# Performance work log

Hardware: AMD Instinct MI355X
Metric: run time of the kernel (lower is better)

Reference implementation:

```python
import jax, jax.numpy as jnp
import numpy as np

H, W, CIN, COUT, B = 56, 56, 64, 64, 32
K = 3            # kernel_size
WIN = 15         # win_range
R = (WIN - 1) // 2


def _make_sample_idx():
    """Per-pixel fixed random sample locations within a WINxWIN window,
    mirroring Dconv_drop.__init__ (random.sample over valid window indices)."""
    rng = np.random.default_rng(0)
    ii = np.arange(H)[:, None, None]          # [H,1,1]
    jj = np.arange(W)[None, :, None]          # [1,W,1]
    lo_i = np.maximum(0, ii - R); hi_i = np.minimum(H - 1, ii + R)
    lo_j = np.maximum(0, jj - R); hi_j = np.minimum(W - 1, jj + R)
    ri = rng.integers(np.broadcast_to(lo_i, (H, W, K * K)),
                      np.broadcast_to(hi_i, (H, W, K * K)) + 1)
    rj = rng.integers(np.broadcast_to(lo_j, (H, W, K * K)),
                      np.broadcast_to(hi_j, (H, W, K * K)) + 1)
    return (ri * W + rj).astype(np.int32)    # [H,W,9] indices into H*W


def setup_inputs() -> dict:
    key = jax.random.key(0)
    k1, k2 = jax.random.split(key)
    x = jax.random.normal(k1, (B, CIN, H, W), dtype=jnp.float32)
    weight = jax.random.normal(k2, (COUT, CIN, K, K), dtype=jnp.float32) * 0.05
    sample_idx = jnp.asarray(_make_sample_idx())
    return {"x": x, "weight": weight, "sample_idx": sample_idx}


def reference(x, weight, sample_idx):
    # x: [B,C,H,W]; sample_idx: [H,W,9] flat indices into H*W.
    # Original: scatter gathered pixels into [B,C,3H,3W] grid, then
    # stride-3 kernel-3 conv => per-pixel contraction over the 9 samples.
    b, c, h, w = x.shape
    x_flat = x.reshape(b, c, h * w)
    gathered = x_flat[:, :, sample_idx]              # [B,C,H,W,9]
    w_flat = weight.reshape(weight.shape[0], c, K * K)  # [O,C,9]
    out = jnp.einsum('bchwk,ock->bohw', gathered, w_flat)
    return out
```

## Files before the change

kernel.cpp:

```cpp
#include <hip/hip_runtime.h>
#include <hip/hip_bf16.h>

#define HH 56
#define WW 56
#define CIN 64
#define COUT 64
#define BATCH 32
#define KK 9
#define HWP (HH*WW)
#define NS 18
#define NTILE 49
#define NBLK (NTILE*BATCH)
#define XT_OFF 73728
#define XSW 33

typedef __attribute__((ext_vector_type(8))) short short8;
typedef __attribute__((ext_vector_type(4))) float float4v;
typedef __attribute__((ext_vector_type(4))) unsigned int uint4v;

__device__ __forceinline__ unsigned short f2bf(float f) {
    union { float f; unsigned u; } v; v.f = f;
    unsigned r = v.u + 0x7FFFu + ((v.u >> 16) & 1u);
    return (unsigned short)(r >> 16);
}

__device__ __forceinline__ void prepack_elem(const float* __restrict__ w,
                                             unsigned short* __restrict__ apack,
                                             int e) {
    int j = e & 7;
    int l = (e >> 3) & 63;
    int ss = e >> 9;
    int mb = ss / 18;
    int s  = ss - mb * 18;
    int o = mb * 16 + (l & 15);
    int c = ((s & 1) << 5) + ((l >> 4) << 3) + j;
    int k = s >> 1;
    apack[e] = f2bf(w[(o * CIN + c) * KK + k]);
}

__global__ __launch_bounds__(256) void prep_kernel(
    const float* __restrict__ x, const float* __restrict__ w,
    unsigned int* __restrict__ xt, unsigned short* __restrict__ apack)
{
    int bid = blockIdx.x;
    int t   = threadIdx.x;
    if (bid < 784) {
        int u   = bid * 256 + t;
        int c2q = u & 7;
        int hq  = u >> 3;
        int b   = hq / 784;
        int q   = hq - b * 784;
        int hw  = q * 4;
        const float* xb = x + ((size_t)b * CIN + c2q * 8) * HWP + hw;
        float4v f[8];
        #pragma unroll
        for (int i = 0; i < 8; ++i)
            f[i] = *(const float4v*)(xb + (size_t)i * HWP);
        unsigned int* xto = xt + ((size_t)b * HWP + hw) * 32 + c2q * 4;
        #pragma unroll
        for (int j = 0; j < 4; ++j) {
            uint4v o;
            #pragma unroll
            for (int ci = 0; ci < 4; ++ci)
                o[ci] = (unsigned)f2bf(f[2 * ci][j]) |
                        ((unsigned)f2bf(f[2 * ci + 1][j]) << 16);
            *(uint4v*)(xto + (size_t)j * 32) = o;
        }
    } else {
        prepack_elem(w, apack, (bid - 784) * 256 + t);
    }
}

__global__ __launch_bounds__(256) void prep_weights_only(
    const float* __restrict__ w, unsigned short* __restrict__ apack)
{
    prepack_elem(w, apack, blockIdx.x * 256 + threadIdx.x);
}

__global__ __launch_bounds__(256, 5) void dconv_main(
    const unsigned int* __restrict__ xt, const int* __restrict__ sidx,
    const unsigned short* __restrict__ apack, float* __restrict__ out)
{
    __shared__ unsigned int xs[496 * 16];

    const int t    = threadIdx.x;
    const int lane = t & 63;
    const int wv   = t >> 6;
    const int mbp  = wv >> 1;
    const int ntp  = wv & 1;
    const int col  = lane & 15;
    const int krow = lane >> 4;

    int bid  = blockIdx.x;
    int orig = (bid & 7) * 196 + (bid >> 3);
    int b    = orig / NTILE;
    int bx   = orig - b * NTILE;
    int ti = bx / 7, tj = bx - (bx / 7) * 7;
    int r0 = ti * 8 - 7; if (r0 < 0) r0 = 0;
    int c0 = tj * 8 - 7; if (c0 < 0) c0 = 0;

    const unsigned int* xtb = xt + (size_t)b * HWP * 32;

    int lb[2][KK];
    #pragma unroll
    for (int nn = 0; nn < 2; ++nn) {
        int p  = (ntp * 2 + nn) * 16 + col;
        int gi = ti * 8 + (p >> 3), gj = tj * 8 + (p & 7);
        const int* sp = sidx + (gi * WW + gj) * KK;
        #pragma unroll
        for (int k = 0; k < KK; ++k) {
            int g  = sp[k];
            int si = g / WW, sj = g - si * WW;
            int row = (si - r0) * 22 + (sj - c0);
            lb[nn][k] = row * 64 + ((krow ^ (row & 3)) << 4);
        }
    }

    const unsigned short* apW = apack + (size_t)(mbp * 2 * NS) * 512 + lane * 8;

    float4v zero = {0.f, 0.f, 0.f, 0.f};
    float4v acc[2][2] = {{zero, zero}, {zero, zero}};
    const char* xsb = (const char*)xs;

    #pragma unroll
    for (int sh = 0; sh < 2; ++sh) {
        for (int grp = wv; grp < 31; grp += 4) {
            int row = grp * 16 + (lane >> 2);
            int rc  = row < 483 ? row : 483;
            int lsr = rc / 22;
            int lsc = rc - lsr * 22;
            int si = r0 + lsr; if (si > HH - 1) si = HH - 1;
            int sj = c0 + lsc; if (sj > WW - 1) sj = WW - 1;
            int q  = (lane & 3) ^ (rc & 3);
            const unsigned int* src =
                xtb + (size_t)(si * WW + sj) * 32 + sh * 16 + (q << 2);
            __builtin_amdgcn_global_load_lds(
                (const __attribute__((address_space(1))) unsigned int*)src,
                (__attribute__((address_space(3))) unsigned int*)(xs + grp * 256),
                16, 0, 0);
        }
        __syncthreads();

        #pragma unroll
        for (int k = 0; k < KK; ++k) {
            short8 a0 = *(const short8*)(apW + (size_t)(2 * k + sh) * 512);
            short8 a1 = *(const short8*)(apW + (size_t)(NS + 2 * k + sh) * 512);
            #pragma unroll
            for (int nn = 0; nn < 2; ++nn) {
                short8 bv = *(const short8*)(xsb + lb[nn][k]);
                acc[0][nn] = __builtin_amdgcn_mfma_f32_16x16x32_bf16(
                    a0, bv, acc[0][nn], 0, 0, 0);
                acc[1][nn] = __builtin_amdgcn_mfma_f32_16x16x32_bf16(
                    a1, bv, acc[1][nn], 0, 0, 0);
            }
        }
        if (sh == 0) __syncthreads();
    }

    float* ob = out + ((size_t)b * COUT + mbp * 32) * HWP;
    #pragma unroll
    for (int m = 0; m < 2; ++m) {
        #pragma unroll
        for (int nn = 0; nn < 2; ++nn) {
            int p = (ntp * 2 + nn) * 16 + col;
            int g = (ti * 8 + (p >> 3)) * WW + tj * 8 + (p & 7);
            #pragma unroll
            for (int r = 0; r < 4; ++r)
                ob[(m * 16 + krow * 4 + r) * HWP + g] = acc[m][nn][r];
        }
    }
}

__global__ __launch_bounds__(256, 2) void dconv_fb(
    const float* __restrict__ x, const int* __restrict__ sidx,
    const unsigned short* __restrict__ apack, float* __restrict__ out)
{
    __shared__ unsigned int xs[484 * XSW];

    const int t    = threadIdx.x;
    const int lane = t & 63;
    const int wv   = t >> 6;
    const int mbp  = wv >> 1;
    const int ntp  = wv & 1;
    const int col  = lane & 15;
    const int krow = lane >> 4;
    const int bx   = blockIdx.x;
    const int b    = blockIdx.y;
    const int ti = bx / 7, tj = bx - (bx / 7) * 7;
    int r0 = ti * 8 - 7; if (r0 < 0) r0 = 0;
    int r1 = ti * 8 + 14; if (r1 > HH - 1) r1 = HH - 1;
    int c0 = tj * 8 - 7; if (c0 < 0) c0 = 0;
    int c1 = tj * 8 + 14; if (c1 > WW - 1) c1 = WW - 1;

    int lb[2][KK];
    #pragma unroll
    for (int nn = 0; nn < 2; ++nn) {
        int p  = (ntp * 2 + nn) * 16 + col;
        int gi = ti * 8 + (p >> 3), gj = tj * 8 + (p & 7);
        const int* sp = sidx + (gi * WW + gj) * KK;
        #pragma unroll
        for (int k = 0; k < KK; ++k) {
            int g  = sp[k];
            int si = g / WW, sj = g - si * WW;
            lb[nn][k] = ((si - r0) * 22 + (sj - c0)) * (XSW * 4);
        }
    }

    short8 areg[2][NS];
    #pragma unroll
    for (int m = 0; m < 2; ++m) {
        const unsigned short* ap = apack + ((mbp * 2 + m) * NS) * 512 + lane * 8;
        #pragma unroll
        for (int s = 0; s < NS; ++s)
            areg[m][s] = *(const short8*)(ap + s * 512);
    }

    const float* xb = x + (size_t)b * CIN * HWP;
    for (int e = t; e < 32 * 512; e += 256) {
        int c2 = e >> 9, ls = e & 511;
        if (ls < 484) {
            int lsr = ls / 22;
            int si = r0 + lsr, sj = c0 + (ls - lsr * 22);
            if (si <= r1 && sj <= c1) {
                int g = si * WW + sj;
                float f0 = xb[(2 * c2) * HWP + g];
                float f1 = xb[(2 * c2 + 1) * HWP + g];
                xs[ls * XSW + c2] =
                    (unsigned)f2bf(f0) | ((unsigned)f2bf(f1) << 16);
            }
        }
    }
    __syncthreads();

    float4v zero = {0.f, 0.f, 0.f, 0.f};
    float4v acc[2][2] = {{zero, zero}, {zero, zero}};
    const char* xsb = (const char*)xs + krow * 16;

    #pragma unroll
    for (int k = 0; k < KK; ++k) {
        #pragma unroll
        for (int nn = 0; nn < 2; ++nn) {
            const char* ba = xsb + lb[nn][k];
            union { int i[4]; short8 s8; } b0, b1;
            #pragma unroll
            for (int w = 0; w < 4; ++w) {
                b0.i[w] = *(const int*)(ba + w * 4);
                b1.i[w] = *(const int*)(ba + 64 + w * 4);
            }
            acc[0][nn] = __builtin_amdgcn_mfma_f32_16x16x32_bf16(
                areg[0][2 * k], b0.s8, acc[0][nn], 0, 0, 0);
            acc[1][nn] = __builtin_amdgcn_mfma_f32_16x16x32_bf16(
                areg[1][2 * k], b0.s8, acc[1][nn], 0, 0, 0);
            acc[0][nn] = __builtin_amdgcn_mfma_f32_16x16x32_bf16(
                areg[0][2 * k + 1], b1.s8, acc[0][nn], 0, 0, 0);
            acc[1][nn] = __builtin_amdgcn_mfma_f32_16x16x32_bf16(
                areg[1][2 * k + 1], b1.s8, acc[1][nn], 0, 0, 0);
        }
    }

    float* ob = out + ((size_t)b * COUT + mbp * 32) * HWP;
    #pragma unroll
    for (int m = 0; m < 2; ++m) {
        #pragma unroll
        for (int nn = 0; nn < 2; ++nn) {
            int p = (ntp * 2 + nn) * 16 + col;
            int g = (ti * 8 + (p >> 3)) * WW + tj * 8 + (p & 7);
            #pragma unroll
            for (int r = 0; r < 4; ++r)
                ob[(m * 16 + krow * 4 + r) * HWP + g] = acc[m][nn][r];
        }
    }
}

extern "C" void kernel_launch(void* const* d_in, const int* in_sizes, int n_in,
                              void* d_out, int out_size, void* d_ws, size_t ws_size,
                              hipStream_t stream) {
    const float* x    = (const float*)d_in[0];
    const float* w    = (const float*)d_in[1];
    const int*   sidx = (const int*)d_in[2];
    float* out = (float*)d_out;
    unsigned short* apack = (unsigned short*)d_ws;
    unsigned int*   xt    = (unsigned int*)((char*)d_ws + XT_OFF);

    size_t need = (size_t)XT_OFF + (size_t)BATCH * HWP * 128;
    if (ws_size >= need) {
        prep_kernel<<<928, 256, 0, stream>>>(x, w, xt, apack);
        dconv_main<<<NBLK, 256, 0, stream>>>(xt, sidx, apack, out);
    } else {
        prep_weights_only<<<144, 256, 0, stream>>>(w, apack);
        dim3 grid(NTILE, BATCH);
        dconv_fb<<<grid, 256, 0, stream>>>(x, sidx, apack, out);
    }
}
```

Baseline: 33.48 us.

## Process two batch images per block to reuse sample indices and weight fragments

Each block of the main conv kernel now handles two batch images for the same spatial tile. It stages both images' halo regions in LDS and reuses the per-lane sample offsets and A-weight fragments across both. This halves the grid and amortizes the index computation and weight loads. In exchange it doubles LDS per block and the accumulator count, and lowers launch bounds occupancy from 5 to 2 blocks per CU.

```diff
diff --git a/kernel.cpp b/kernel.cpp
--- a/kernel.cpp
+++ b/kernel.cpp
@@ -10,9 +10,10 @@
 #define HWP (HH*WW)
 #define NS 18
 #define NTILE 49
-#define NBLK (NTILE*BATCH)
+#define NBLK2 784
 #define XT_OFF 73728
 #define XSW 33
+#define REGW 7936
 
 typedef __attribute__((ext_vector_type(8))) short short8;
 typedef __attribute__((ext_vector_type(4))) float float4v;
@@ -77,11 +78,11 @@
     prepack_elem(w, apack, blockIdx.x * 256 + threadIdx.x);
 }
 
-__global__ __launch_bounds__(256, 5) void dconv_main(
+__global__ __launch_bounds__(256, 2) void dconv_main(
     const unsigned int* __restrict__ xt, const int* __restrict__ sidx,
     const unsigned short* __restrict__ apack, float* __restrict__ out)
 {
-    __shared__ unsigned int xs[496 * 16];
+    __shared__ unsigned int xs[2 * REGW];
 
     const int t    = threadIdx.x;
     const int lane = t & 63;
@@ -92,14 +93,15 @@
     const int krow = lane >> 4;
 
     int bid  = blockIdx.x;
-    int orig = (bid & 7) * 196 + (bid >> 3);
-    int b    = orig / NTILE;
-    int bx   = orig - b * NTILE;
+    int orig = (bid & 7) * 98 + (bid >> 3);
+    int bp   = orig / NTILE;
+    int bx   = orig - bp * NTILE;
+    int b0   = bp * 2;
     int ti = bx / 7, tj = bx - (bx / 7) * 7;
     int r0 = ti * 8 - 7; if (r0 < 0) r0 = 0;
     int c0 = tj * 8 - 7; if (c0 < 0) c0 = 0;
 
-    const unsigned int* xtb = xt + (size_t)b * HWP * 32;
+    const unsigned int* xtb0 = xt + (size_t)b0 * HWP * 32;
 
     int lb[2][KK];
     #pragma unroll
@@ -119,13 +121,22 @@
     const unsigned short* apW = apack + (size_t)(mbp * 2 * NS) * 512 + lane * 8;
 
     float4v zero = {0.f, 0.f, 0.f, 0.f};
-    float4v acc[2][2] = {{zero, zero}, {zero, zero}};
+    float4v acc[2][2][2];
+    #pragma unroll
+    for (int m = 0; m < 2; ++m)
+        #pragma unroll
+        for (int ba = 0; ba < 2; ++ba)
+            #pragma unroll
+            for (int nn = 0; nn < 2; ++nn)
+                acc[m][ba][nn] = zero;
     const char* xsb = (const char*)xs;
 
     #pragma unroll
     for (int sh = 0; sh < 2; ++sh) {
-        for (int grp = wv; grp < 31; grp += 4) {
-            int row = grp * 16 + (lane >> 2);
+        for (int grp = wv; grp < 62; grp += 4) {
+            int ba   = grp < 31 ? 0 : 1;
+            int rgrp = grp - ba * 31;
+            int row = rgrp * 16 + (lane >> 2);
             int rc  = row < 483 ? row : 483;
             int lsr = rc / 22;
             int lsc = rc - lsr * 22;
@@ -133,10 +144,12 @@
             int sj = c0 + lsc; if (sj > WW - 1) sj = WW - 1;
             int q  = (lane & 3) ^ (rc & 3);
             const unsigned int* src =
-                xtb + (size_t)(si * WW + sj) * 32 + sh * 16 + (q << 2);
+                xtb0 + (size_t)ba * HWP * 32 +
+                (size_t)(si * WW + sj) * 32 + sh * 16 + (q << 2);
             __builtin_amdgcn_global_load_lds(
                 (const __attribute__((address_space(1))) unsigned int*)src,
-                (__attribute__((address_space(3))) unsigned int*)(xs + grp * 256),
+                (__attribute__((address_space(3))) unsigned int*)
+                    (xs + ba * REGW + rgrp * 256),
                 16, 0, 0);
         }
         __syncthreads();
@@ -146,27 +159,33 @@
             short8 a0 = *(const short8*)(apW + (size_t)(2 * k + sh) * 512);
             short8 a1 = *(const short8*)(apW + (size_t)(NS + 2 * k + sh) * 512);
             #pragma unroll
+            for (int ba = 0; ba < 2; ++ba) {
+                #pragma unroll
+                for (int nn = 0; nn < 2; ++nn) {
+                    short8 bv = *(const short8*)(xsb + ba * (REGW * 4) + lb[nn][k]);
+                    acc[0][ba][nn] = __builtin_amdgcn_mfma_f32_16x16x32_bf16(
+                        a0, bv, acc[0][ba][nn], 0, 0, 0);
+                    acc[1][ba][nn] = __builtin_amdgcn_mfma_f32_16x16x32_bf16(
+                        a1, bv, acc[1][ba][nn], 0, 0, 0);
+                }
+            }
+        }
+        if (sh == 0) __syncthreads();
+    }
+
+    #pragma unroll
+    for (int ba = 0; ba < 2; ++ba) {
+        float* ob = out + ((size_t)(b0 + ba) * COUT + mbp * 32) * HWP;
+        #pragma unroll
+        for (int m = 0; m < 2; ++m) {
+            #pragma unroll
             for (int nn = 0; nn < 2; ++nn) {
-                short8 bv = *(const short8*)(xsb + lb[nn][k]);
-                acc[0][nn] = __builtin_amdgcn_mfma_f32_16x16x32_bf16(
-                    a0, bv, acc[0][nn], 0, 0, 0);
-                acc[1][nn] = __builtin_amdgcn_mfma_f32_16x16x32_bf16(
-                    a1, bv, acc[1][nn], 0, 0, 0);
+                int p = (ntp * 2 + nn) * 16 + col;
+                int g = (ti * 8 + (p >> 3)) * WW + tj * 8 + (p & 7);
+                #pragma unroll
+                for (int r = 0; r < 4; ++r)
+                    ob[(m * 16 + krow * 4 + r) * HWP + g] = acc[m][ba][nn][r];
             }
-        }
-        if (sh == 0) __syncthreads();
-    }
-
-    float* ob = out + ((size_t)b * COUT + mbp * 32) * HWP;
-    #pragma unroll
-    for (int m = 0; m < 2; ++m) {
-        #pragma unroll
-        for (int nn = 0; nn < 2; ++nn) {
-            int p = (ntp * 2 + nn) * 16 + col;
-            int g = (ti * 8 + (p >> 3)) * WW + tj * 8 + (p & 7);
-            #pragma unroll
-            for (int r = 0; r < 4; ++r)
-                ob[(m * 16 + krow * 4 + r) * HWP + g] = acc[m][nn][r];
         }
     }
 }
@@ -285,7 +304,7 @@
     size_t need = (size_t)XT_OFF + (size_t)BATCH * HWP * 128;
     if (ws_size >= need) {
         prep_kernel<<<928, 256, 0, stream>>>(x, w, xt, apack);
-        dconv_main<<<NBLK, 256, 0, stream>>>(xt, sidx, apack, out);
+        dconv_main<<<NBLK2, 256, 0, stream>>>(xt, sidx, apack, out);
     } else {
         prep_weights_only<<<144, 256, 0, stream>>>(w, apack);
         dim3 grid(NTILE, BATCH);
```

Result: slower. 34.47 us (+2.9%).
